# Kernel optimization log

Measured on AMD Instinct MI355X. Metric: run time of the kernel, lower is better.

Reference implementation:

```python
import jax, jax.numpy as jnp
import numpy as np

HEADS = 16


def setup_inputs() -> dict:
    key = jax.random.key(0)
    ks = jax.random.split(key, 6)
    B, S, D = 2, 2048, 1024
    return {
        "x": jax.random.normal(ks[0], (B, S, D), dtype=jnp.float32),
        "q_in": jax.random.normal(ks[1], (B, S, D), dtype=jnp.float32),
        "WQ": jax.random.normal(ks[2], (D, D), dtype=jnp.float32) * 0.03,
        "WK": jax.random.normal(ks[3], (D, D), dtype=jnp.float32) * 0.03,
        "WV": jax.random.normal(ks[4], (D, D), dtype=jnp.float32) * 0.03,
        "WO": jax.random.normal(ks[5], (D, D), dtype=jnp.float32) * 0.03,
    }


def reference(x, q_in, WQ, WK, WV, WO):
    B, S, D = x.shape
    H = HEADS
    hd = D // H
    # projections; tf.split on last dim == reshape to (B,S,H,hd)
    Q = (q_in @ WQ).reshape(B, S, H, hd)
    K = (x @ WK).reshape(B, S, H, hd)
    V = (x @ WV).reshape(B, S, H, hd)
    scores = jnp.einsum("bqhd,bkhd->bhqk", Q, K)  # [B,H,S,S]
    # causal additive mask: 0 on/below diagonal, -inf above
    causal = jnp.tril(jnp.ones((S, S), dtype=bool))
    mask = jnp.where(causal, 0.0, -jnp.inf).astype(scores.dtype)
    # NOTE: original adds the mask BEFORE scaling, and scales by sqrt(d_model)
    attn = jax.nn.softmax((scores + mask) / np.sqrt(D).astype(scores.dtype), axis=-1)
    ctx = jnp.einsum("bhqk,bkhd->bqhd", attn, V).reshape(B, S, D)
    return ctx @ WO
```

## Files before the change

kernel.cpp:

```cpp
#include <hip/hip_runtime.h>


typedef __bf16 bf16_t;
typedef __attribute__((ext_vector_type(8))) __bf16 bf16x8;
typedef __attribute__((ext_vector_type(4))) __bf16 bf16x4;
typedef __attribute__((ext_vector_type(4))) float f32x4;

#define SCALE_LOG2E 0.045084220027780106f
#define FIXED_MAX 8.0f

__device__ __forceinline__ void async_load16(const void* g, void* l) {
  __builtin_amdgcn_global_load_lds(
      (const __attribute__((address_space(1))) void*)g,
      (__attribute__((address_space(3))) void*)l, 16, 0, 0);
}

__global__ void prep(const float* __restrict__ x, const float* __restrict__ q,
                     const float* __restrict__ w0, const float* __restrict__ w1,
                     const float* __restrict__ w2, const float* __restrict__ w3,
                     bf16_t* __restrict__ xb, bf16_t* __restrict__ qb,
                     bf16_t* __restrict__ wt) {
  const int bid = blockIdx.x;
  if (bid < 4096) {
    const float* src = (bid >= 2048) ? q : x;
    bf16_t* dst = (bid >= 2048) ? qb : xb;
    const size_t i = ((size_t)(bid & 2047) * 256 + threadIdx.x) * 8;
    float4 v0 = *(const float4*)(src + i);
    float4 v1 = *(const float4*)(src + i + 4);
    bf16x8 o;
    o[0] = (bf16_t)v0.x; o[1] = (bf16_t)v0.y; o[2] = (bf16_t)v0.z; o[3] = (bf16_t)v0.w;
    o[4] = (bf16_t)v1.x; o[5] = (bf16_t)v1.y; o[6] = (bf16_t)v1.z; o[7] = (bf16_t)v1.w;
    *(bf16x8*)(dst + i) = o;
  } else {
    const int wb = bid - 4096;
    const int z = wb >> 8;
    const float* W = z == 0 ? w0 : z == 1 ? w1 : z == 2 ? w2 : w3;
    bf16_t* dst = wt + (size_t)z * 1048576;
    const int r0 = ((wb >> 4) & 15) * 64, c0 = (wb & 15) * 64;
    __shared__ bf16_t t[64][72];
#pragma unroll
    for (int i = 0; i < 16; ++i) {
      int flat = i * 256 + threadIdx.x;
      int r = flat >> 6, c = flat & 63;
      t[c][r] = (bf16_t)W[(size_t)(r0 + r) * 1024 + c0 + c];
    }
    __syncthreads();
    const int c = threadIdx.x >> 2, seg = (threadIdx.x & 3) * 16;
    bf16x8 a = *(const bf16x8*)&t[c][seg];
    bf16x8 b = *(const bf16x8*)&t[c][seg + 8];
    bf16_t* drow = dst + (size_t)(c0 + c) * 1024 + r0 + seg;
    *(bf16x8*)drow = a;
    *(bf16x8*)(drow + 8) = b;
  }
}

template <int MODE>
__global__ __launch_bounds__(256, MODE == 2 ? 4 : 2) void gemm128(
    const bf16_t* __restrict__ Aq, const bf16_t* __restrict__ Ax,
    const bf16_t* __restrict__ Bt,
    bf16_t* __restrict__ Cq, bf16_t* __restrict__ Cvt, float* __restrict__ Cf) {
  constexpr int K = 1024;
  constexpr int NT = (MODE == 2) ? 2 : 4;
  constexpr int NROWS = NT * 32;
  const int n0 = blockIdx.x * NROWS;
  const int m0 = blockIdx.y * 128;
  const bf16_t* A = (MODE == 0 && n0 >= 1024) ? Ax : Aq;

  __shared__ bf16_t lA[128 * 32];
  __shared__ bf16_t lB[NROWS * 32];

  const int tid = threadIdx.x;
  const int w = tid >> 6, l = tid & 63;
  const int wm = (w & 1) * 64, wn = (w >> 1) * (NT * 16);
  const int sr = l >> 2;
  const int sk = (l & 3) * 8;
  const int fr = l & 15, fc = (l >> 4) * 8;

  f32x4 acc[4][NT] = {};

  for (int kt = 0; kt < K; kt += 32) {
    __syncthreads();
#pragma unroll
    for (int c = 0; c < 2; ++c) {
      const int ch = w * 2 + c;
      async_load16(A + (size_t)(m0 + ch * 16 + sr) * K + kt + sk, &lA[ch * 512]);
      if (NT == 4 || c == 0) {
        const int bch = (NT == 4) ? ch : w;
        async_load16(Bt + (size_t)(n0 + bch * 16 + sr) * K + kt + sk, &lB[bch * 512]);
      }
    }
    __syncthreads();
    bf16x8 af[4], bfr[NT];
#pragma unroll
    for (int i = 0; i < 4; ++i) af[i] = *(const bf16x8*)&lA[(wm + i * 16 + fr) * 32 + fc];
#pragma unroll
    for (int j = 0; j < NT; ++j) bfr[j] = *(const bf16x8*)&lB[(wn + j * 16 + fr) * 32 + fc];
#pragma unroll
    for (int i = 0; i < 4; ++i)
#pragma unroll
      for (int j = 0; j < NT; ++j)
        acc[i][j] = __builtin_amdgcn_mfma_f32_16x16x32_bf16(af[i], bfr[j], acc[i][j], 0, 0, 0);
  }

  if (MODE == 2) {
#pragma unroll
    for (int i = 0; i < 4; ++i) {
      const int m = m0 + wm + i * 16 + (l >> 4) * 4;
#pragma unroll
      for (int j = 0; j < NT; ++j) {
        const int n = n0 + wn + j * 16 + fr;
#pragma unroll
        for (int r = 0; r < 4; ++r) Cf[(size_t)(m + r) * 1024 + n] = acc[i][j][r];
      }
    }
  } else if (n0 < 2048) {
#pragma unroll
    for (int i = 0; i < 4; ++i) {
      const int m = m0 + wm + i * 16 + (l >> 4) * 4;
#pragma unroll
      for (int j = 0; j < NT; ++j) {
        const int n = n0 + wn + j * 16 + fr;
#pragma unroll
        for (int r = 0; r < 4; ++r) Cq[(size_t)(m + r) * 3072 + n] = (bf16_t)acc[i][j][r];
      }
    }
  } else {
#pragma unroll
    for (int i = 0; i < 4; ++i) {
      const int mb = m0 + wm + i * 16 + (l >> 4) * 4;
      const int bb = mb >> 11, ss = mb & 2047;
#pragma unroll
      for (int j = 0; j < NT; ++j) {
        const int nn = n0 - 2048 + wn + j * 16 + fr;
        const int hh = nn >> 6, dd = nn & 63;
        bf16x4 pk;
#pragma unroll
        for (int r = 0; r < 4; ++r) pk[r] = (bf16_t)acc[i][j][r];
        *(bf16x4*)(Cvt + (size_t)((bb * 16 + hh) * 64 + dd) * 2048 + ss) = pk;
      }
    }
  }
}

__global__ __launch_bounds__(256, 2) void attn64p(const bf16_t* __restrict__ qkv,
                                                  const bf16_t* __restrict__ vt,
                                                  bf16_t* __restrict__ ctx) {
  const int p = blockIdx.y;
  const int bh = blockIdx.x;
  const int b = bh >> 4, h = bh & 15;
  const int tid = threadIdx.x, w = tid >> 6, l = tid & 63;
  const int fr = l & 15, fq = l >> 4;

  __shared__ __align__(16) bf16_t lK[2][64 * 64];
  __shared__ __align__(16) bf16_t lV[2][64 * 64];
  __shared__ __align__(16) bf16_t lP[4][16 * 72];

  const bf16_t* kg = qkv + (size_t)b * 2048 * 3072 + 1024 + h * 64;
  const bf16_t* vg = vt + (size_t)(b * 16 + h) * 64 * 2048;

  const int srow = l >> 3;
  const int swz = ((l & 7) ^ srow) * 8;
  const int xr = fr & 7;

  bf16x8 ones;
#pragma unroll
  for (int i = 0; i < 8; ++i) ones[i] = (bf16_t)1.0f;

#pragma unroll 1
  for (int phase = 0; phase < 2; ++phase) {
    const int qt = (phase == 0) ? (16 + p) : (15 - p);
    const int q0 = qt * 64;
    const int qw = q0 + w * 16;
    const int ktmax = qt;

    bf16x8 qf[2];
#pragma unroll
    for (int ks = 0; ks < 2; ++ks)
      qf[ks] = *(const bf16x8*)(qkv + (size_t)(b * 2048 + qw + fr) * 3072 +
                                h * 64 + ks * 32 + fq * 8);

    f32x4 o[4] = {};
    f32x4 liacc = {};

    if (phase == 1) __syncthreads();
#pragma unroll
    for (int c = 0; c < 2; ++c) {
      const int row = w * 16 + c * 8 + srow;
      async_load16(kg + (size_t)row * 3072 + swz, &lK[0][(w * 16 + c * 8) * 64]);
      async_load16(vg + (size_t)row * 2048 + swz, &lV[0][(w * 16 + c * 8) * 64]);
    }

    for (int kt = 0; kt <= ktmax; ++kt) {
      const int buf = kt & 1;
      __syncthreads();
      if (kt < ktmax) {
#pragma unroll
        for (int c = 0; c < 2; ++c) {
          const int row = w * 16 + c * 8 + srow;
          async_load16(kg + (size_t)((kt + 1) * 64 + row) * 3072 + swz,
                       &lK[buf ^ 1][(w * 16 + c * 8) * 64]);
          async_load16(vg + (size_t)row * 2048 + (kt + 1) * 64 + swz,
                       &lV[buf ^ 1][(w * 16 + c * 8) * 64]);
        }
      }

      f32x4 s[4] = {};
#pragma unroll
      for (int t = 0; t < 4; ++t)
#pragma unroll
        for (int ks = 0; ks < 2; ++ks) {
          bf16x8 kf = *(const bf16x8*)&lK[buf][(t * 16 + fr) * 64 + ((ks * 4 + fq) ^ xr) * 8];
          s[t] = __builtin_amdgcn_mfma_f32_16x16x32_bf16(kf, qf[ks], s[t], 0, 0, 0);
        }

      const int kbase = kt * 64;
      const int qq = qw + fr;
      const bool needmask = (kbase + 63) > qw;
#pragma unroll
      for (int t = 0; t < 4; ++t) {
        bf16x4 pk;
#pragma unroll
        for (int r = 0; r < 4; ++r) {
          float v = fmaf(s[t][r], SCALE_LOG2E, -FIXED_MAX);
          if (needmask && (kbase + t * 16 + fq * 4 + r > qq)) v = -1e30f;
          pk[r] = (bf16_t)__builtin_amdgcn_exp2f(v);
        }
        *(bf16x4*)&lP[w][fr * 72 + t * 16 + fq * 4] = pk;
      }

      bf16x8 pf[2];
#pragma unroll
      for (int g = 0; g < 2; ++g)
        pf[g] = *(const bf16x8*)&lP[w][fr * 72 + g * 32 + fq * 8];
#pragma unroll
      for (int g = 0; g < 2; ++g) {
#pragma unroll
        for (int dt = 0; dt < 4; ++dt) {
          bf16x8 vf = *(const bf16x8*)&lV[buf][(dt * 16 + fr) * 64 + ((g * 4 + fq) ^ xr) * 8];
          o[dt] = __builtin_amdgcn_mfma_f32_16x16x32_bf16(vf, pf[g], o[dt], 0, 0, 0);
        }
        liacc = __builtin_amdgcn_mfma_f32_16x16x32_bf16(ones, pf[g], liacc, 0, 0, 0);
      }
    }

    const float inv = 1.f / liacc[0];
    bf16_t* cb = ctx + (size_t)(b * 2048 + qw + fr) * 1024 + h * 64;
#pragma unroll
    for (int dt = 0; dt < 4; ++dt) {
      bf16x4 ov;
#pragma unroll
      for (int r = 0; r < 4; ++r) ov[r] = (bf16_t)(o[dt][r] * inv);
      *(bf16x4*)(cb + dt * 16 + fq * 4) = ov;
    }
  }
}

extern "C" void kernel_launch(void* const* d_in, const int* in_sizes, int n_in,
                              void* d_out, int out_size, void* d_ws, size_t ws_size,
                              hipStream_t stream) {
  const float* x  = (const float*)d_in[0];
  const float* q  = (const float*)d_in[1];
  const float* WQ = (const float*)d_in[2];
  const float* WK = (const float*)d_in[3];
  const float* WV = (const float*)d_in[4];
  const float* WO = (const float*)d_in[5];
  float* out = (float*)d_out;

  bf16_t* qb  = (bf16_t*)d_ws;
  bf16_t* xb  = qb + 4194304;
  bf16_t* wt  = xb + 4194304;
  bf16_t* qkv = wt + 4194304;
  bf16_t* vtp = qkv + (size_t)4096 * 3072;
  bf16_t* ctx = vtp + 4194304;

  prep<<<dim3(5120), 256, 0, stream>>>(x, q, WQ, WK, WV, WO, xb, qb, wt);
  gemm128<0><<<dim3(24, 32), 256, 0, stream>>>(qb, xb, wt, qkv, vtp, nullptr);
  attn64p<<<dim3(32, 16), 256, 0, stream>>>(qkv, vtp, ctx);
  gemm128<2><<<dim3(16, 32), 256, 0, stream>>>(ctx, ctx, wt + (size_t)3072 * 1024,
                                               nullptr, nullptr, out);
}
```

Measured before the change: 193.6 us.

## Split attention key tiles across 8 waves with LDS reduction of partial outputs

The attention kernel now runs 512 threads per block. Eight waves each handle a 16-query slice paired with one half of the 64-key tile, and waves whose key half lies fully above the causal diagonal skip the compute. Partial outputs and row sums from the second key half are reduced through a new LDS buffer before normalization, which aims to raise wave-level parallelism and MFMA occupancy per CU. The cost is the extra reduction, the added barriers and more LDS use. Separately, the occupancy hint on the QKV GEMM is raised from 2 to 3 blocks, which may force register pressure or spills.

```diff
diff --git a/kernel.cpp b/kernel.cpp
--- a/kernel.cpp
+++ b/kernel.cpp
@@ -55,7 +55,7 @@
 }
 
 template <int MODE>
-__global__ __launch_bounds__(256, MODE == 2 ? 4 : 2) void gemm128(
+__global__ __launch_bounds__(256, MODE == 2 ? 4 : 3) void gemm128(
     const bf16_t* __restrict__ Aq, const bf16_t* __restrict__ Ax,
     const bf16_t* __restrict__ Bt,
     bf16_t* __restrict__ Cq, bf16_t* __restrict__ Cvt, float* __restrict__ Cf) {
@@ -142,18 +142,21 @@
   }
 }
 
-__global__ __launch_bounds__(256, 2) void attn64p(const bf16_t* __restrict__ qkv,
-                                                  const bf16_t* __restrict__ vt,
-                                                  bf16_t* __restrict__ ctx) {
+__global__ __launch_bounds__(512, 4) void attn8w(const bf16_t* __restrict__ qkv,
+                                                 const bf16_t* __restrict__ vt,
+                                                 bf16_t* __restrict__ ctx) {
   const int p = blockIdx.y;
   const int bh = blockIdx.x;
   const int b = bh >> 4, h = bh & 15;
   const int tid = threadIdx.x, w = tid >> 6, l = tid & 63;
   const int fr = l & 15, fq = l >> 4;
+  const int qq4 = w & 3;
+  const int kh = w >> 2;
 
   __shared__ __align__(16) bf16_t lK[2][64 * 64];
   __shared__ __align__(16) bf16_t lV[2][64 * 64];
-  __shared__ __align__(16) bf16_t lP[4][16 * 72];
+  __shared__ __align__(16) bf16_t lP[8][16 * 40];
+  __shared__ __align__(16) float lRed[4][16][68];
 
   const bf16_t* kg = qkv + (size_t)b * 2048 * 3072 + 1024 + h * 64;
   const bf16_t* vg = vt + (size_t)(b * 16 + h) * 64 * 2048;
@@ -170,8 +173,7 @@
   for (int phase = 0; phase < 2; ++phase) {
     const int qt = (phase == 0) ? (16 + p) : (15 - p);
     const int q0 = qt * 64;
-    const int qw = q0 + w * 16;
-    const int ktmax = qt;
+    const int qw = q0 + qq4 * 16;
 
     bf16x8 qf[2];
 #pragma unroll
@@ -182,75 +184,77 @@
     f32x4 o[4] = {};
     f32x4 liacc = {};
 
-    if (phase == 1) __syncthreads();
-#pragma unroll
-    for (int c = 0; c < 2; ++c) {
-      const int row = w * 16 + c * 8 + srow;
-      async_load16(kg + (size_t)row * 3072 + swz, &lK[0][(w * 16 + c * 8) * 64]);
-      async_load16(vg + (size_t)row * 2048 + swz, &lV[0][(w * 16 + c * 8) * 64]);
-    }
-
-    for (int kt = 0; kt <= ktmax; ++kt) {
+    {
+      const int row = w * 8 + srow;
+      async_load16(kg + (size_t)row * 3072 + swz, &lK[0][w * 512]);
+      async_load16(vg + (size_t)row * 2048 + swz, &lV[0][w * 512]);
+    }
+
+    for (int kt = 0; kt <= qt; ++kt) {
       const int buf = kt & 1;
       __syncthreads();
-      if (kt < ktmax) {
-#pragma unroll
-        for (int c = 0; c < 2; ++c) {
-          const int row = w * 16 + c * 8 + srow;
-          async_load16(kg + (size_t)((kt + 1) * 64 + row) * 3072 + swz,
-                       &lK[buf ^ 1][(w * 16 + c * 8) * 64]);
-          async_load16(vg + (size_t)row * 2048 + (kt + 1) * 64 + swz,
-                       &lV[buf ^ 1][(w * 16 + c * 8) * 64]);
-        }
-      }
-
-      f32x4 s[4] = {};
-#pragma unroll
-      for (int t = 0; t < 4; ++t)
+      if (kt < qt) {
+        const int row = w * 8 + srow;
+        async_load16(kg + (size_t)((kt + 1) * 64 + row) * 3072 + swz, &lK[buf ^ 1][w * 512]);
+        async_load16(vg + (size_t)row * 2048 + (kt + 1) * 64 + swz, &lV[buf ^ 1][w * 512]);
+      }
+
+      const int kb = kt * 64 + kh * 32;
+      if (kb > qw + 15) continue;
+
+      f32x4 s[2] = {};
+#pragma unroll
+      for (int t = 0; t < 2; ++t)
 #pragma unroll
         for (int ks = 0; ks < 2; ++ks) {
-          bf16x8 kf = *(const bf16x8*)&lK[buf][(t * 16 + fr) * 64 + ((ks * 4 + fq) ^ xr) * 8];
+          bf16x8 kf = *(const bf16x8*)&lK[buf][(kh * 32 + t * 16 + fr) * 64 +
+                                              ((ks * 4 + fq) ^ xr) * 8];
           s[t] = __builtin_amdgcn_mfma_f32_16x16x32_bf16(kf, qf[ks], s[t], 0, 0, 0);
         }
 
-      const int kbase = kt * 64;
       const int qq = qw + fr;
-      const bool needmask = (kbase + 63) > qw;
-#pragma unroll
-      for (int t = 0; t < 4; ++t) {
+      const bool needmask = (kb + 31) > qw;
+#pragma unroll
+      for (int t = 0; t < 2; ++t) {
         bf16x4 pk;
 #pragma unroll
         for (int r = 0; r < 4; ++r) {
           float v = fmaf(s[t][r], SCALE_LOG2E, -FIXED_MAX);
-          if (needmask && (kbase + t * 16 + fq * 4 + r > qq)) v = -1e30f;
+          if (needmask && (kb + t * 16 + fq * 4 + r > qq)) v = -1e30f;
           pk[r] = (bf16_t)__builtin_amdgcn_exp2f(v);
         }
-        *(bf16x4*)&lP[w][fr * 72 + t * 16 + fq * 4] = pk;
-      }
-
-      bf16x8 pf[2];
-#pragma unroll
-      for (int g = 0; g < 2; ++g)
-        pf[g] = *(const bf16x8*)&lP[w][fr * 72 + g * 32 + fq * 8];
-#pragma unroll
-      for (int g = 0; g < 2; ++g) {
-#pragma unroll
-        for (int dt = 0; dt < 4; ++dt) {
-          bf16x8 vf = *(const bf16x8*)&lV[buf][(dt * 16 + fr) * 64 + ((g * 4 + fq) ^ xr) * 8];
-          o[dt] = __builtin_amdgcn_mfma_f32_16x16x32_bf16(vf, pf[g], o[dt], 0, 0, 0);
-        }
-        liacc = __builtin_amdgcn_mfma_f32_16x16x32_bf16(ones, pf[g], liacc, 0, 0, 0);
-      }
-    }
-
-    const float inv = 1.f / liacc[0];
-    bf16_t* cb = ctx + (size_t)(b * 2048 + qw + fr) * 1024 + h * 64;
-#pragma unroll
-    for (int dt = 0; dt < 4; ++dt) {
-      bf16x4 ov;
-#pragma unroll
-      for (int r = 0; r < 4; ++r) ov[r] = (bf16_t)(o[dt][r] * inv);
-      *(bf16x4*)(cb + dt * 16 + fq * 4) = ov;
+        *(bf16x4*)&lP[w][fr * 40 + t * 16 + fq * 4] = pk;
+      }
+
+      bf16x8 pf = *(const bf16x8*)&lP[w][fr * 40 + fq * 8];
+#pragma unroll
+      for (int dt = 0; dt < 4; ++dt) {
+        bf16x8 vf = *(const bf16x8*)&lV[buf][(dt * 16 + fr) * 64 + ((kh * 4 + fq) ^ xr) * 8];
+        o[dt] = __builtin_amdgcn_mfma_f32_16x16x32_bf16(vf, pf, o[dt], 0, 0, 0);
+      }
+      liacc = __builtin_amdgcn_mfma_f32_16x16x32_bf16(ones, pf, liacc, 0, 0, 0);
+    }
+
+    __syncthreads();
+    if (kh) {
+#pragma unroll
+      for (int dt = 0; dt < 4; ++dt)
+        *(f32x4*)&lRed[qq4][fr][dt * 16 + fq * 4] = o[dt];
+      if (fq == 0) lRed[qq4][fr][64] = liacc[0];
+    }
+    __syncthreads();
+    if (!kh) {
+      const float lsum = liacc[0] + lRed[qq4][fr][64];
+      const float inv = 1.f / lsum;
+      bf16_t* cb = ctx + (size_t)(b * 2048 + qw + fr) * 1024 + h * 64;
+#pragma unroll
+      for (int dt = 0; dt < 4; ++dt) {
+        f32x4 v = o[dt] + *(f32x4*)&lRed[qq4][fr][dt * 16 + fq * 4];
+        bf16x4 ov;
+#pragma unroll
+        for (int r = 0; r < 4; ++r) ov[r] = (bf16_t)(v[r] * inv);
+        *(bf16x4*)(cb + dt * 16 + fq * 4) = ov;
+      }
     }
   }
 }
@@ -275,7 +279,7 @@
 
   prep<<<dim3(5120), 256, 0, stream>>>(x, q, WQ, WK, WV, WO, xb, qb, wt);
   gemm128<0><<<dim3(24, 32), 256, 0, stream>>>(qb, xb, wt, qkv, vtp, nullptr);
-  attn64p<<<dim3(32, 16), 256, 0, stream>>>(qkv, vtp, ctx);
+  attn8w<<<dim3(32, 16), 512, 0, stream>>>(qkv, vtp, ctx);
   gemm128<2><<<dim3(16, 32), 256, 0, stream>>>(ctx, ctx, wt + (size_t)3072 * 1024,
                                                nullptr, nullptr, out);
 }
```

Measured after the change: 188.3 us. 1.03x faster.
